# Kernel tuning notes

Hardware: AMD Instinct MI355X
Metric: run time of the kernel (lower is better)

## Reference

```python
import jax, jax.numpy as jnp
import numpy as np

N_ELEMENTS = 64  # StructureElementLayer(n_elements=64)


def setup_inputs() -> dict:
    key = jax.random.key(0)
    k1, k2 = jax.random.split(key)
    # x: [N, C, T, V] skeleton sequence (batch, coord channels, time, joints)
    x = jax.random.normal(k1, (256, 3, 256, 25), dtype=jnp.float32)
    # StructureElementLayer parameters (torch.rand init / ones*3 init)
    centres = jax.random.uniform(k2, (N_ELEMENTS, 2), dtype=jnp.float32)
    sharpness = jnp.ones((N_ELEMENTS, 2), dtype=jnp.float32) * 3.0
    return {"x": x, "centres": centres, "sharpness": sharpness}


def _mst_deaths(D):
    """Dim-0 Vietoris-Rips persistence deaths == MST edge weights (Prim's algorithm).

    D: [n, n] symmetric distance matrix. Returns [n-1] finite death values
    (births are all 0; the single essential (0, inf) pair contributes
    exp(-inf)=0 to the structure-element layer and is dropped).
    """
    n = D.shape[0]
    in_tree = jnp.zeros((n,), dtype=bool).at[0].set(True)
    dist = D[0]  # min distance from each node to the current tree

    def step(carry, _):
        in_tree, dist = carry
        d = jnp.where(in_tree, jnp.inf, dist)
        j = jnp.argmin(d)
        w = d[j]
        in_tree = in_tree.at[j].set(True)
        dist = jnp.minimum(dist, D[j])
        return (in_tree, dist), w

    (_, _), deaths = jax.lax.scan(step, (in_tree, dist), None, length=n - 1)
    return deaths


def _forward(x, centres, sharpness):
    xm = x.mean(1)                                  # [N, T, V]
    diff = xm[..., :, None] - xm[..., None, :]      # [N, T, V, V] pairwise joint diffs
    diff = diff.mean(-3)                            # [N, V, V]
    feat = jnp.linalg.norm(diff, axis=1)            # [N, V]  (torch.norm(., 2, dim=1))
    feat = (feat - feat.min()) / (feat.max() - feat.min())
    # Euclidean distance matrix of the N points in V-dim space (grad-safe sqrt)
    sq = jnp.sum(feat * feat, axis=1)
    D2 = sq[:, None] + sq[None, :] - 2.0 * (feat @ feat.T)
    D2 = jnp.maximum(D2, 0.0)
    D = jnp.where(D2 > 0.0, jnp.sqrt(jnp.where(D2 > 0.0, D2, 1.0)), 0.0)
    deaths = _mst_deaths(D)                         # [N-1]
    diag = jnp.stack([jnp.zeros_like(deaths), deaths], axis=-1)  # [N-1, 2] (birth, death)
    # StructureElementLayer: sum_i exp(-sum_d (p_id - c_kd)^2 * s_kd^2)
    d2 = (diag[:, None, :] - centres[None, :, :]) ** 2            # [N-1, K, 2]
    out = jnp.exp(-(d2 * (sharpness ** 2)).sum(-1)).sum(0)        # [K]
    return out


def reference(x, centres, sharpness):
    return _forward(x, centres, sharpness)
```

## Files before the change

### kernel.cpp

```cpp
#include <hip/hip_runtime.h>
#include <hip/hip_fp16.h>


#define WS_FEAT 0
#define WS_FMN  26624
#define WS_FMX  27648
#define WS_RK   28672
#define WS_DTH  29696
#define WS_NCDC 30720
#define WS_D16  65536
#define WS_MP   196608

#define INF32 0xFFFFFFFFu
#define SA 132

__global__ void __launch_bounds__(256) k_feat(const float* __restrict__ x,
                                              float* __restrict__ featG,
                                              float* __restrict__ fmnG,
                                              float* __restrict__ fmxG,
                                              unsigned int* __restrict__ Mp) {
    __shared__ float sums[25];
    __shared__ float mrow[25];
    __shared__ float S12[2];
    __shared__ unsigned int bmn, bmx;
    const int n = blockIdx.x;
    const int tid = threadIdx.x;
    if (tid < 66) Mp[n * 66 + tid] = INF32;
    if (tid < 25) sums[tid] = 0.0f;
    if (tid == 0) { bmn = 0x7F800000u; bmx = 0u; }
    __syncthreads();
    if (tid < 200) {
        const float* base = x + (long)n * 19200 + 4 * tid;
        float a0 = 0.f, a1 = 0.f, a2 = 0.f, a3 = 0.f;
        #pragma unroll
        for (int i = 0; i < 24; ++i) {
            float4 v = *reinterpret_cast<const float4*>(base + 800 * i);
            a0 += v.x; a1 += v.y; a2 += v.z; a3 += v.w;
        }
        const int v0 = (4 * tid) % 25;
        atomicAdd(&sums[v0], a0);
        atomicAdd(&sums[(v0 + 1) % 25], a1);
        atomicAdd(&sums[(v0 + 2) % 25], a2);
        atomicAdd(&sums[(v0 + 3) % 25], a3);
    }
    __syncthreads();
    if (tid < 25) mrow[tid] = sums[tid] * (1.0f / 768.0f);
    __syncthreads();
    if (tid == 0) {
        float S1 = 0.f, S2 = 0.f;
        #pragma unroll
        for (int v = 0; v < 25; ++v) { S1 += mrow[v]; S2 += mrow[v] * mrow[v]; }
        S12[0] = S1; S12[1] = S2;
    }
    __syncthreads();
    if (tid < 25) {
        const float r = mrow[tid];
        float q = S12[1] - 2.f * r * S12[0] + 25.f * r * r;
        q = fmaxf(q, 0.f);
        const float f = sqrtf(q);
        featG[n * 26 + tid] = f;
        atomicMin(&bmn, __float_as_uint(f));
        atomicMax(&bmx, __float_as_uint(f));
    }
    __syncthreads();
    if (tid == 0) { fmnG[n] = __uint_as_float(bmn); fmxG[n] = __uint_as_float(bmx); }
}

template <int CTRL>
__device__ __forceinline__ unsigned int dpp_min_step(unsigned int v) {
    unsigned int t = (unsigned int)__builtin_amdgcn_update_dpp(
        (int)0xFFFFFFFF, (int)v, CTRL, 0xF, 0xF, false);
    return (t < v) ? t : v;
}

__global__ void __launch_bounds__(256) k_dist(const float* __restrict__ featG,
                                              unsigned short* __restrict__ D16,
                                              unsigned int* __restrict__ rowKeyG) {
    __shared__ float featS[6656];
    __shared__ unsigned int wred[4];
    const int i = blockIdx.x;
    const int t = threadIdx.x;
    #pragma unroll
    for (int it = 0; it < 7; ++it) {
        const int o = it * 256 + t;
        if (o < 1664) reinterpret_cast<float4*>(featS)[o] =
            reinterpret_cast<const float4*>(featG)[o];
    }
    __syncthreads();
    float fi[25];
    #pragma unroll
    for (int v = 0; v < 25; ++v) fi[v] = featS[i * 26 + v];
    float s = 0.f;
    #pragma unroll
    for (int v = 0; v < 25; ++v) {
        const float d = fi[v] - featS[t * 26 + v];
        s += d * d;
    }
    const unsigned int w16 = (unsigned int)__half_as_ushort(__float2half(s));
    D16[i * 256 + t] = (unsigned short)w16;
    const unsigned int lo = (t < i) ? t : i, hi = (t < i) ? i : t;
    unsigned int key = (t == i) ? INF32 : ((w16 << 16) | (lo << 8) | hi);
    key = dpp_min_step<0x111>(key);
    key = dpp_min_step<0x112>(key);
    key = dpp_min_step<0x114>(key);
    key = dpp_min_step<0x118>(key);
    key = dpp_min_step<0x142>(key);
    key = dpp_min_step<0x143>(key);
    if ((t & 63) == 63) wred[t >> 6] = key;
    __syncthreads();
    if (t == 0) {
        const unsigned int b0 = wred[0] < wred[1] ? wred[0] : wred[1];
        const unsigned int b1 = wred[2] < wred[3] ? wred[2] : wred[3];
        rowKeyG[i] = b0 < b1 ? b0 : b1;
    }
}

template <bool RECORD>
__device__ __forceinline__ void wave0_phase(int n, int lane,
        unsigned int* rowKeyS, unsigned char* parentS, unsigned char* newidS,
        unsigned char* cmapS, float* deaths, unsigned int* ncS, unsigned int* dcS) {
    unsigned int par[4];
    #pragma unroll
    for (int s = 0; s < 4; ++s) {
        const int i = lane + 64 * s;
        if (i < n) {
            const unsigned int rk = rowKeyS[i];
            const unsigned int u = (rk >> 8) & 0xFFu, v = rk & 0xFFu;
            unsigned int p = (u == (unsigned int)i) ? v : u;
            if (rk == INF32) p = (unsigned int)i;
            par[s] = p;
            parentS[i] = (unsigned char)p;
        }
    }
    #pragma unroll
    for (int s = 0; s < 4; ++s) {
        const int i = lane + 64 * s;
        if (i < n) {
            const unsigned int p = par[s];
            if (p != (unsigned int)i) {
                if (parentS[p] == (unsigned char)i && (unsigned int)i < p) {
                    parentS[i] = (unsigned char)i;
                } else if (RECORD) {
                    const unsigned int d = atomicAdd(dcS, 1u);
                    const unsigned int rk = rowKeyS[i];
                    deaths[d] = sqrtf(__half2float(__ushort_as_half(
                        (unsigned short)(rk >> 16))));
                }
            }
        }
    }
    for (;;) {
        bool ch = false;
        #pragma unroll
        for (int s = 0; s < 4; ++s) {
            const int i = lane + 64 * s;
            if (i < n) {
                const unsigned char p0 = parentS[i];
                const unsigned char np = parentS[p0];
                if (np != p0) { ch = true; parentS[i] = np; }
            }
        }
        if (__ballot(ch) == 0ull) break;
    }
    bool isr[4];
    #pragma unroll
    for (int s = 0; s < 4; ++s) {
        const int i = lane + 64 * s;
        isr[s] = (i < n) && (parentS[i] == (unsigned char)i);
    }
    unsigned int base = 0;
    const unsigned long long below = (1ull << lane) - 1ull;
    #pragma unroll
    for (int s = 0; s < 4; ++s) {
        const unsigned long long mask = __ballot(isr[s]);
        if (isr[s]) {
            const int i = lane + 64 * s;
            newidS[i] = (unsigned char)(base + __popcll(mask & below));
        }
        base += (unsigned int)__popcll(mask);
    }
    if (lane == 0) *ncS = base;
    #pragma unroll
    for (int s = 0; s < 4; ++s) {
        const int i = lane + 64 * s;
        if (i < n) cmapS[i] = newidS[parentS[i]];
    }
}

__global__ void __launch_bounds__(256) k_contract(const unsigned short* __restrict__ D16g,
                                                  const unsigned int* __restrict__ rowKeyG,
                                                  unsigned int* __restrict__ Mp,
                                                  float* __restrict__ deathsG,
                                                  unsigned int* __restrict__ ncdcG) {
    __shared__ unsigned int rowKeyS[256];
    __shared__ unsigned char parentS[256], newidS[256], cmapS[256];
    __shared__ unsigned int ncS, dcS;
    __shared__ float deathsS[256];
    const int tid = threadIdx.x;
    const int b = blockIdx.x;
    rowKeyS[tid] = rowKeyG[tid];
    if (tid == 0) dcS = 0;
    __syncthreads();
    if (tid < 64) {
        if (b == 0)
            wave0_phase<true>(256, tid, rowKeyS, parentS, newidS, cmapS,
                              deathsS, &ncS, &dcS);
        else
            wave0_phase<false>(256, tid, rowKeyS, parentS, newidS, cmapS,
                               nullptr, &ncS, nullptr);
    }
    __syncthreads();
    if (b == 0) {
        if (tid < dcS) deathsG[tid] = deathsS[tid];
        if (tid == 0) { ncdcG[0] = ncS; ncdcG[1] = dcS; }
    }
    const unsigned int ca = cmapS[b];
    const unsigned int cb = cmapS[tid];
    if (ca != cb) {
        const unsigned int w16 = (unsigned int)D16g[b * 256 + tid];
        const unsigned int lo = ca < cb ? ca : cb;
        const unsigned int hi = ca < cb ? cb : ca;
        atomicMin(&Mp[ca * SA + cb], (w16 << 16) | (lo << 8) | hi);
    }
}

__global__ void __launch_bounds__(1024) k_mst(const unsigned int* __restrict__ Mp,
                                              const float* __restrict__ deathsG,
                                              const unsigned int* __restrict__ ncdcG,
                                              const float* __restrict__ fmnG,
                                              const float* __restrict__ fmxG,
                                              const float* __restrict__ centres,
                                              const float* __restrict__ sharp,
                                              float* __restrict__ out) {
    __shared__ unsigned int Mb[128 * SA];
    __shared__ float deathsS[256];
    __shared__ unsigned int mmS[2];
    __shared__ float outpart[1024];
    __shared__ unsigned int ncS, dcS;
    const int tid = threadIdx.x;
    const int wv = tid >> 6, lane = tid & 63;

    if (tid == 0) {
        ncS = ncdcG[0]; dcS = ncdcG[1];
        mmS[0] = 0x7F800000u; mmS[1] = 0u;
    }
    if (tid < 256) deathsS[tid] = deathsG[tid];
    __syncthreads();
    const int nc = (int)ncS;
    for (int idx = tid; idx < nc * SA; idx += 1024) Mb[idx] = Mp[idx];
    if (wv == 15) {
        #pragma unroll
        for (int q = 0; q < 4; ++q) {
            const int j = lane * 4 + q;
            atomicMin(&mmS[0], __float_as_uint(fmnG[j]));
            atomicMax(&mmS[1], __float_as_uint(fmxG[j]));
        }
    }
    __syncthreads();

    if (wv == 0) {
        const int dc = (int)dcS;
        unsigned int d0 = (Mb[lane]      & 0xFFFF0000u) | (unsigned)lane;
        unsigned int d1 = (Mb[64 + lane] & 0xFFFF0000u) | (unsigned)(64 + lane);
        unsigned int tb = 0;
        if (lane == 0) { tb = 1u; d0 = INF32; }
        for (int it = 0; it < nc - 1; ++it) {
            unsigned int key = d0 < d1 ? d0 : d1;
            key = dpp_min_step<0x111>(key);
            key = dpp_min_step<0x112>(key);
            key = dpp_min_step<0x114>(key);
            key = dpp_min_step<0x118>(key);
            key = dpp_min_step<0x142>(key);
            key = dpp_min_step<0x143>(key);
            const unsigned int best =
                (unsigned int)__builtin_amdgcn_readlane((int)key, 63);
            const unsigned int j = best & 0xFFu;
            if (lane == 0)
                deathsS[dc + it] = sqrtf(__half2float(__ushort_as_half(
                    (unsigned short)(best >> 16))));
            const unsigned int lj = j & 63u, slot = j >> 6;
            if ((unsigned)lane == lj) {
                tb |= (1u << slot);
                if (slot == 0u) d0 = INF32; else d1 = INF32;
            }
            const unsigned int rb = j * SA;
            const unsigned int n0 = (Mb[rb + lane]      & 0xFFFF0000u) | (unsigned)lane;
            const unsigned int n1 = (Mb[rb + 64 + lane] & 0xFFFF0000u) | (unsigned)(64 + lane);
            d0 = (tb & 1u) ? INF32 : (n0 < d0 ? n0 : d0);
            d1 = (tb & 2u) ? INF32 : (n1 < d1 ? n1 : d1);
        }
    }
    __syncthreads();

    const float mn = __uint_as_float(mmS[0]);
    const float mx = __uint_as_float(mmS[1]);
    const float inv = 1.0f / (mx - mn);
    const int k = tid & 63;
    const int part = tid >> 6;
    const float c0 = centres[2 * k], c1 = centres[2 * k + 1];
    const float s0 = sharp[2 * k],   s1 = sharp[2 * k + 1];
    const float t0 = c0 * c0 * s0 * s0;
    const float s1sq = s1 * s1;
    float acc = 0.f;
    for (int idx = part; idx < 255; idx += 16) {
        const float d = deathsS[idx] * inv - c1;
        acc += __expf(-(t0 + d * d * s1sq));
    }
    outpart[tid] = acc;
    __syncthreads();
    if (tid < 64) {
        float s = 0.f;
        #pragma unroll
        for (int pp = 0; pp < 16; ++pp) s += outpart[tid + 64 * pp];
        out[tid] = s;
    }
}

extern "C" void kernel_launch(void* const* d_in, const int* in_sizes, int n_in,
                              void* d_out, int out_size, void* d_ws, size_t ws_size,
                              hipStream_t stream) {
    const float* x       = (const float*)d_in[0];
    const float* centres = (const float*)d_in[1];
    const float* sharp   = (const float*)d_in[2];
    float* out = (float*)d_out;
    char* ws = (char*)d_ws;
    float*          featG = (float*)(ws + WS_FEAT);
    float*          fmnG  = (float*)(ws + WS_FMN);
    float*          fmxG  = (float*)(ws + WS_FMX);
    unsigned int*   rk    = (unsigned int*)(ws + WS_RK);
    float*          dth   = (float*)(ws + WS_DTH);
    unsigned int*   ncdc  = (unsigned int*)(ws + WS_NCDC);
    unsigned short* D16   = (unsigned short*)(ws + WS_D16);
    unsigned int*   Mp    = (unsigned int*)(ws + WS_MP);

    k_feat<<<256, 256, 0, stream>>>(x, featG, fmnG, fmxG, Mp);
    k_dist<<<256, 256, 0, stream>>>(featG, D16, rk);
    k_contract<<<256, 256, 0, stream>>>(D16, rk, Mp, dth, ncdc);
    k_mst<<<1, 1024, 0, stream>>>(Mp, dth, ncdc, fmnG, fmxG, centres, sharp, out);
}
```

Measured before the change: 112.9 us.

## Replace serial Prim loop in final MST stage with parallel Boruvka contraction rounds

Swaps the single-wave sequential Prim iteration over the contracted component graph for repeated Boruvka rounds in the final kernel. Each round finds per-component minimum edges with all threads, merges components through a shared helper, and rebuilds a smaller contracted adjacency matrix in a ping-pong shared buffer with atomicMin. This aims to remove the long serial dependency chain of nc-1 wave reductions, at the cost of more barriers, shared memory and atomics per round.

```diff
diff --git a/kernel.cpp b/kernel.cpp
--- a/kernel.cpp
+++ b/kernel.cpp
@@ -13,6 +13,8 @@
 
 #define INF32 0xFFFFFFFFu
 #define SA 132
+#define SB 68
+#define OFF_B (128 * SA)
 
 __global__ void __launch_bounds__(256) k_feat(const float* __restrict__ x,
                                               float* __restrict__ featG,
@@ -232,11 +234,13 @@
                                               const float* __restrict__ centres,
                                               const float* __restrict__ sharp,
                                               float* __restrict__ out) {
-    __shared__ unsigned int Mb[128 * SA];
-    __shared__ float deathsS[256];
+    __shared__ unsigned int Mb[128 * SA + 64 * SB];
+    __shared__ unsigned int rowKeyS[256];
+    __shared__ unsigned char parentS[256], newidS[256], cmapS[256];
+    __shared__ unsigned int ncS, dcS;
+    __shared__ float deaths[256];
     __shared__ unsigned int mmS[2];
     __shared__ float outpart[1024];
-    __shared__ unsigned int ncS, dcS;
     const int tid = threadIdx.x;
     const int wv = tid >> 6, lane = tid & 63;
 
@@ -244,10 +248,11 @@
         ncS = ncdcG[0]; dcS = ncdcG[1];
         mmS[0] = 0x7F800000u; mmS[1] = 0u;
     }
-    if (tid < 256) deathsS[tid] = deathsG[tid];
-    __syncthreads();
-    const int nc = (int)ncS;
-    for (int idx = tid; idx < nc * SA; idx += 1024) Mb[idx] = Mp[idx];
+    if (tid < 256) deaths[tid] = deathsG[tid];
+    __syncthreads();
+    int n = (int)ncS;
+
+    for (int idx = tid; idx < n * SA; idx += 1024) Mb[idx] = Mp[idx];
     if (wv == 15) {
         #pragma unroll
         for (int q = 0; q < 4; ++q) {
@@ -258,39 +263,50 @@
     }
     __syncthreads();
 
-    if (wv == 0) {
-        const int dc = (int)dcS;
-        unsigned int d0 = (Mb[lane]      & 0xFFFF0000u) | (unsigned)lane;
-        unsigned int d1 = (Mb[64 + lane] & 0xFFFF0000u) | (unsigned)(64 + lane);
-        unsigned int tb = 0;
-        if (lane == 0) { tb = 1u; d0 = INF32; }
-        for (int it = 0; it < nc - 1; ++it) {
-            unsigned int key = d0 < d1 ? d0 : d1;
-            key = dpp_min_step<0x111>(key);
-            key = dpp_min_step<0x112>(key);
-            key = dpp_min_step<0x114>(key);
-            key = dpp_min_step<0x118>(key);
-            key = dpp_min_step<0x142>(key);
-            key = dpp_min_step<0x143>(key);
-            const unsigned int best =
-                (unsigned int)__builtin_amdgcn_readlane((int)key, 63);
-            const unsigned int j = best & 0xFFu;
-            if (lane == 0)
-                deathsS[dc + it] = sqrtf(__half2float(__ushort_as_half(
-                    (unsigned short)(best >> 16))));
-            const unsigned int lj = j & 63u, slot = j >> 6;
-            if ((unsigned)lane == lj) {
-                tb |= (1u << slot);
-                if (slot == 0u) d0 = INF32; else d1 = INF32;
+    int srcOff = 0, srcStr = SA, dstOff = OFF_B, dstStr = SB;
+    for (int round = 0; round < 12 && n > 1; ++round) {
+        if (tid < n) rowKeyS[tid] = INF32;
+        __syncthreads();
+        if (tid < 8 * n) {
+            const int a = tid >> 3, sub = tid & 7;
+            const unsigned int* row = &Mb[srcOff + a * srcStr];
+            unsigned int best = INF32;
+            for (int b2 = sub; b2 < n; b2 += 8) {
+                const unsigned int v = row[b2];
+                best = v < best ? v : best;
             }
-            const unsigned int rb = j * SA;
-            const unsigned int n0 = (Mb[rb + lane]      & 0xFFFF0000u) | (unsigned)lane;
-            const unsigned int n1 = (Mb[rb + 64 + lane] & 0xFFFF0000u) | (unsigned)(64 + lane);
-            d0 = (tb & 1u) ? INF32 : (n0 < d0 ? n0 : d0);
-            d1 = (tb & 2u) ? INF32 : (n1 < d1 ? n1 : d1);
-        }
-    }
-    __syncthreads();
+            if (best != INF32) atomicMin(&rowKeyS[a], best);
+        }
+        __syncthreads();
+        if (tid < 64)
+            wave0_phase<true>(n, tid, rowKeyS, parentS, newidS, cmapS,
+                              deaths, &ncS, &dcS);
+        __syncthreads();
+        const int nc = (int)ncS;
+        if (nc > 1) {
+            for (int w = tid; w < nc * dstStr; w += 1024) Mb[dstOff + w] = INF32;
+            __syncthreads();
+            if (tid < 8 * n) {
+                const int a = tid >> 3, sub = tid & 7;
+                const unsigned int ca = cmapS[a];
+                const unsigned int* row = &Mb[srcOff + a * srcStr];
+                for (int b2 = sub; b2 < n; b2 += 8) {
+                    const unsigned int cb = cmapS[b2];
+                    const unsigned int v = row[b2];
+                    if (ca != cb && v != INF32) {
+                        const unsigned int lo = ca < cb ? ca : cb;
+                        const unsigned int hi = ca < cb ? cb : ca;
+                        atomicMin(&Mb[dstOff + ca * dstStr + cb],
+                                  (v & 0xFFFF0000u) | (lo << 8) | hi);
+                    }
+                }
+            }
+            __syncthreads();
+        }
+        const int t1 = srcOff; srcOff = dstOff; dstOff = t1;
+        const int t2 = srcStr; srcStr = dstStr; dstStr = t2;
+        n = nc;
+    }
 
     const float mn = __uint_as_float(mmS[0]);
     const float mx = __uint_as_float(mmS[1]);
@@ -303,7 +319,7 @@
     const float s1sq = s1 * s1;
     float acc = 0.f;
     for (int idx = part; idx < 255; idx += 16) {
-        const float d = deathsS[idx] * inv - c1;
+        const float d = deaths[idx] * inv - c1;
         acc += __expf(-(t0 + d * d * s1sq));
     }
     outpart[tid] = acc;
```

Measured after the change: 106.5 us. 5.7% less time.
